# Optimization experiments

Measured on AMD Instinct MI355X. Metric: run time of the kernel, lower is better.

The kernel has to match this reference:

```python
import jax, jax.numpy as jnp
import numpy as np


def setup_inputs() -> dict:
    key = jax.random.key(0)
    ks = jax.random.split(key, 9)
    B, T, S, E, H = 4, 4096, 4096, 512, 64
    return {
        "x": jax.random.normal(ks[0], (B, T, 1), dtype=jnp.float32),
        "tok_emb": jax.random.normal(ks[1], (B, S, E), dtype=jnp.float32),
        "key_w": jax.random.normal(ks[2], (H, E), dtype=jnp.float32) * 0.05,
        "key_b": jax.random.normal(ks[3], (H,), dtype=jnp.float32) * 0.05,
        "query_w": jax.random.normal(ks[4], (H, 1), dtype=jnp.float32) * 0.05,
        "query_b": jax.random.normal(ks[5], (H,), dtype=jnp.float32) * 0.05,
        "value_w": jax.random.normal(ks[6], (H, E), dtype=jnp.float32) * 0.05,
        "proj_w": jax.random.normal(ks[7], (1, H), dtype=jnp.float32) * 0.05,
        "proj_b": jax.random.normal(ks[8], (1,), dtype=jnp.float32) * 0.05,
    }


def reference(x, tok_emb, key_w, key_b, query_w, query_b, value_w, proj_w, proj_b):
    # k = tanh(Linear(tok_emb))            [B,S,H]
    k = jnp.tanh(jnp.einsum("bse,he->bsh", tok_emb, key_w) + key_b)
    # q = tanh(Linear(x)); x last dim is 1 [B,T,H]
    q = jnp.tanh(jnp.einsum("btu,hu->bth", x, query_w) + query_b)
    scale = k.shape[-1] ** (-0.5)
    wei = jnp.einsum("bth,bsh->bts", q, k) * scale  # [B,T,S]
    # NOTE: softmax over dim=-2 (the query/T axis), faithful to the original
    wei = jax.nn.softmax(wei, axis=-2)
    v = jnp.tanh(jnp.einsum("bse,he->bsh", tok_emb, value_w))  # [B,S,H]
    out = jnp.tanh(jnp.einsum("bts,bsh->bth", wei, v))         # [B,T,H]
    out = jnp.einsum("bth,oh->bto", out, proj_w) + proj_b      # [B,T,1]
    return jnp.squeeze(out, axis=-1)                            # [B,T]
```

## Files before the change

### kernel.cpp

```cpp
#include <hip/hip_runtime.h>
#include <math.h>

#define BB 4
#define TT 4096
#define SS 4096
#define EE 512
#define HH 64
#define NN 128
#define XR 6.0f


typedef __attribute__((ext_vector_type(8))) __bf16 bf16x8;
typedef __attribute__((ext_vector_type(16))) float f32x16;

__device__ __forceinline__ unsigned short f2b(float f) {
  unsigned int u = __float_as_uint(f);
  return (unsigned short)((u + 0x7FFFu + ((u >> 16) & 1u)) >> 16);
}

__device__ __forceinline__ float fast_tanh(float v) {
  float e = __expf(fminf(60.0f, 2.0f * v));
  return (e - 1.0f) * __builtin_amdgcn_rcpf(e + 1.0f);
}

__global__ __launch_bounds__(256) void prep_sm_kernel(
    const float* __restrict__ kw, const float* __restrict__ vw,
    const float* __restrict__ qw, const float* __restrict__ qb,
    const float* __restrict__ x, unsigned int* __restrict__ Wfrag,
    float* __restrict__ Cmat, unsigned short* __restrict__ qnA,
    float* __restrict__ Sm_part, float* __restrict__ Oz) {
  const int blk = blockIdx.x;
  if (blk < 64) {
    int idx = blk * 256 + threadIdx.x;
    int jq = idx & 1;
    int l = (idx >> 1) & 63;
    int ks = (idx >> 7) & 31;
    int nb = idx >> 12;
    int n = nb * 32 + (l & 31);
    int k = ks * 16 + (l >> 5) * 8 + jq * 4;
    const float* row = (n < HH) ? (kw + n * EE + k) : (vw + (n - HH) * EE + k);
    float4 wv = *(const float4*)row;
    Wfrag[idx * 2] = (unsigned int)f2b(wv.x) | ((unsigned int)f2b(wv.y) << 16);
    Wfrag[idx * 2 + 1] =
        (unsigned int)f2b(wv.z) | ((unsigned int)f2b(wv.w) << 16);
  } else if (blk < 128) {
    int idx = (blk - 64) * 256 + threadIdx.x;
    int m = idx >> 7;
    int j = idx & (NN - 1);
    int k = (m * (2 * j + 1)) & 511;
    if (k >= 256) k -= 512;
    Cmat[idx] = cosf((float)k * (float)(M_PI / 256.0));
    if (idx < 8192) ((float4*)Oz)[idx] = make_float4(0.f, 0.f, 0.f, 0.f);
    if (idx < 8192) {
      int h = idx & 63;
      int j2 = idx >> 6;
      float th = (float)M_PI * ((float)j2 + 0.5f) * (1.0f / NN);
      float xj = XR * cosf(th);
      float val = tanhf(fmaf(xj, qw[h], qb[h]));
      int pos =
          (((j2 >> 5) * 4 + (h >> 4)) * 64 + (j2 & 31) + 32 * ((h >> 3) & 1)) *
              8 +
          (h & 7);
      qnA[pos] = f2b(val);
    }
  } else {
    __shared__ float Tm[128][NN + 1];
    int blk2 = blk - 128;
    int b = blk2 >> 5;
    int chunk = blk2 & 31;
    int tid = threadIdx.x;
    if (tid < 128) {
      float xh = x[b * TT + chunk * 128 + tid] * (1.0f / XR);
      xh = fminf(1.0f, fmaxf(-1.0f, xh));
      Tm[tid][0] = 1.0f;
      Tm[tid][1] = xh;
      float x2 = 2.0f * xh;
      float tm2 = 1.0f, tm1 = xh;
#pragma unroll 6
      for (int m = 2; m < NN; ++m) {
        float t = fmaf(x2, tm1, -tm2);
        Tm[tid][m] = t;
        tm2 = tm1;
        tm1 = t;
      }
    }
    __syncthreads();
    if (tid < 128) {
      float s = 0.f;
#pragma unroll 8
      for (int i = 0; i < 128; ++i) s += Tm[i][tid];
      Sm_part[(b * 32 + chunk) * NN + tid] = s;
    }
  }
}

__global__ __launch_bounds__(512) void kvattn_kernel(
    const float* __restrict__ emb, const float* __restrict__ kb,
    const unsigned int* __restrict__ Wfrag, const unsigned short* __restrict__ qnA,
    const float* __restrict__ Cmat, const float* __restrict__ Sm_part,
    float* __restrict__ O) {
  __shared__ __align__(16) char smem[69120];
  unsigned short* A_lds = (unsigned short*)smem;
  unsigned short* ktB = (unsigned short*)smem;
  unsigned short* vB = (unsigned short*)(smem + 8192);
  unsigned short* eA = (unsigned short*)(smem + 16384);
  float* zred = (float*)(smem + 65536);
  float* wql = (float*)(smem + 67840);
  float* izl = (float*)(smem + 68352);
  float* sml = (float*)(smem + 68608);

  const int tid = threadIdx.x;
  const int row0 = blockIdx.x * 64;
  const int bb = row0 >> 12;

  {
    int m = tid >> 3;
    int c8 = tid & 7;
    const float* src = emb + (size_t)(row0 + m) * EE;
    unsigned short* dst = A_lds + (m >> 5) * 16384;
    int ml = m & 31;
    float4 buf[16];
#pragma unroll
    for (int it = 0; it < 16; ++it)
      buf[it] = *(const float4*)(src + (c8 + it * 8) * 4);
#pragma unroll
    for (int it = 0; it < 16; ++it) {
      int k = (c8 + it * 8) * 4;
      float4 v = buf[it];
      int kstep = k >> 4;
      int lane_f = ml + 32 * ((k >> 3) & 1);
      int j = k & 7;
      unsigned int lo = (unsigned int)f2b(v.x) | ((unsigned int)f2b(v.y) << 16);
      unsigned int hi = (unsigned int)f2b(v.z) | ((unsigned int)f2b(v.w) << 16);
      *(uint2*)&dst[(kstep * 64 + lane_f) * 8 + j] = make_uint2(lo, hi);
    }
  }
  if (tid < 128) {
    float s = 0.f;
#pragma unroll 8
    for (int c = 0; c < 32; ++c) s += Sm_part[(bb * 32 + c) * NN + tid];
    sml[tid] = s * ((tid == 0) ? (1.0f / NN) : (2.0f / NN));
  }
  __syncthreads();
  if (tid < 128) {
    float a0 = 0.f, a1 = 0.f, a2 = 0.f, a3 = 0.f;
#pragma unroll
    for (int m = 0; m < NN; m += 4) {
      a0 = fmaf(sml[m], Cmat[m * NN + tid], a0);
      a1 = fmaf(sml[m + 1], Cmat[(m + 1) * NN + tid], a1);
      a2 = fmaf(sml[m + 2], Cmat[(m + 2) * NN + tid], a2);
      a3 = fmaf(sml[m + 3], Cmat[(m + 3) * NN + tid], a3);
    }
    wql[tid] = (a0 + a1) + (a2 + a3);
  }

  const int w8 = tid >> 6;
  const int lane = tid & 63;
  const int w = w8 & 3;
  const int mh = w8 >> 2;
  f32x16 acc = {};
  const bf16x8* Bf = (const bf16x8*)Wfrag;
  const unsigned short* Ah = A_lds + mh * 16384;
#pragma unroll 4
  for (int kstep = 0; kstep < 32; ++kstep) {
    bf16x8 bfr = Bf[(w * 32 + kstep) * 64 + lane];
    bf16x8 a = *(const bf16x8*)&Ah[(kstep * 64 + lane) * 8];
    acc = __builtin_amdgcn_mfma_f32_32x32x16_bf16(a, bfr, acc, 0, 0, 0);
  }
  __syncthreads();

  {
    const int n = w * 32 + (lane & 31);
    if (w < 2) {
      float kbv = kb[n];
      const int ks_h = n >> 4;
      const int off_h = 32 * ((n >> 3) & 1);
      const int jj_h = n & 7;
#pragma unroll
      for (int reg = 0; reg < 16; ++reg) {
        int sl = (reg & 3) + 8 * (reg >> 2) + 4 * (lane >> 5);
        ktB[((mh * 4 + ks_h) * 64 + sl + off_h) * 8 + jj_h] =
            f2b(fast_tanh(acc[reg] + kbv));
      }
    } else {
      int h = n - 64;
      const int nb_h = h >> 5;
      const int lm = h & 31;
#pragma unroll
      for (int reg = 0; reg < 16; ++reg) {
        int sl = (reg & 3) + 8 * (reg >> 2) + 4 * (lane >> 5);
        int s = mh * 32 + sl;
        vB[((nb_h * 4 + (s >> 4)) * 64 + lm + 32 * ((s >> 3) & 1)) * 8 +
           (s & 7)] = f2b(fast_tanh(acc[reg]));
      }
    }
  }
  __syncthreads();

  f32x16 l0 = {};
#pragma unroll
  for (int ks = 0; ks < 4; ++ks) {
    bf16x8 a = *(const bf16x8*)(qnA + ((w * 4 + ks) * 64 + lane) * 8);
    bf16x8 b0 = *(const bf16x8*)&ktB[((mh * 4 + ks) * 64 + lane) * 8];
    l0 = __builtin_amdgcn_mfma_f32_32x32x16_bf16(a, b0, l0, 0, 0, 0);
  }
  float e0[16];
  float zp = 0.f;
#pragma unroll
  for (int r = 0; r < 4; ++r) {
    float4 wq4 = *(const float4*)&wql[w * 32 + 8 * r + 4 * (lane >> 5)];
    float wa[4] = {wq4.x, wq4.y, wq4.z, wq4.w};
#pragma unroll
    for (int c = 0; c < 4; ++c) {
      int reg = 4 * r + c;
      e0[reg] = __expf(l0[reg] * 0.125f);
      zp = fmaf(wa[c], e0[reg], zp);
    }
  }
  zred[(mh * 32 + (lane & 31)) * 9 + w * 2 + (lane >> 5)] = zp;
  __syncthreads();
  if (tid < 64) {
    float sum = 0.f;
#pragma unroll
    for (int k = 0; k < 8; ++k) sum += zred[tid * 9 + k];
    izl[tid] = 1.0f / sum;
  }
  __syncthreads();

  {
    const int s = mh * 32 + (lane & 31);
    const float iz = izl[s];
    const int q0 = w * 4 + (s >> 4);
    const int lof = 32 * ((s >> 3) & 1);
    const int idx = s & 7;
#pragma unroll
    for (int reg = 0; reg < 16; ++reg) {
      int jl = (reg & 3) + 8 * (reg >> 2) + 4 * (lane >> 5);
      eA[(q0 * 64 + jl + lof) * 8 + idx] = f2b(e0[reg] * iz);
    }
  }
  __syncthreads();
  f32x16 o0 = {};
#pragma unroll
  for (int ks = 0; ks < 4; ++ks) {
    bf16x8 a = *(const bf16x8*)&eA[((w * 4 + ks) * 64 + lane) * 8];
    bf16x8 b0 = *(const bf16x8*)&vB[((mh * 4 + ks) * 64 + lane) * 8];
    o0 = __builtin_amdgcn_mfma_f32_32x32x16_bf16(a, b0, o0, 0, 0, 0);
  }
  float* op = O + (size_t)bb * (NN * HH);
  const int h0 = mh * 32 + (lane & 31);
#pragma unroll
  for (int reg = 0; reg < 16; ++reg) {
    int j = w * 32 + (reg & 3) + 8 * (reg >> 2) + 4 * (lane >> 5);
    atomicAdd(&op[j * HH + h0], o0[reg]);
  }
}

__global__ __launch_bounds__(256) void final_kernel(
    const float* __restrict__ x, const float* __restrict__ O,
    const float* __restrict__ pw, const float* __restrict__ pb,
    const float* __restrict__ Cmat, float* __restrict__ y) {
  const int idx = blockIdx.x * 256 + threadIdx.x;
  const int b = idx >> 12;
  __shared__ float yl[NN];
  __shared__ float c[NN];
  {
    const int j = threadIdx.x >> 1;
    const int half = threadIdx.x & 1;
    const float4* Ov =
        (const float4*)(O + ((size_t)(b * NN + j) * HH + half * 32));
    const float4* pwv = (const float4*)(pw + half * 32);
    float s = 0.f;
#pragma unroll
    for (int q = 0; q < 8; ++q) {
      float4 ov = Ov[q];
      float4 pv = pwv[q];
      s += fast_tanh(ov.x) * pv.x + fast_tanh(ov.y) * pv.y +
           fast_tanh(ov.z) * pv.z + fast_tanh(ov.w) * pv.w;
    }
    s += __shfl_xor(s, 1, 64);
    if (half == 0) yl[j] = s + pb[0];
  }
  __syncthreads();
  if (threadIdx.x < NN) {
    int m = threadIdx.x;
    double acc = 0.0;
#pragma unroll 8
    for (int j = 0; j < NN; ++j)
      acc += (double)yl[j] * (double)Cmat[m * NN + j];
    c[m] = (float)(acc * ((m == 0 ? 1.0 : 2.0) / NN));
  }
  __syncthreads();
  float xf = x[idx] * (1.0f / XR);
  xf = fminf(1.0f, fmaxf(-1.0f, xf));
  double xh = (double)xf;
  double b1 = 0.0, b2 = 0.0;
  for (int m = NN - 1; m >= 1; --m) {
    double t = fma(2.0 * xh, b1, (double)c[m] - b2);
    b2 = b1;
    b1 = t;
  }
  y[idx] = (float)fma(xh, b1, (double)c[0] - b2);
}

extern "C" void kernel_launch(void* const* d_in, const int* in_sizes, int n_in,
                              void* d_out, int out_size, void* d_ws,
                              size_t ws_size, hipStream_t stream) {
  const float* x = (const float*)d_in[0];
  const float* emb = (const float*)d_in[1];
  const float* kw = (const float*)d_in[2];
  const float* kb = (const float*)d_in[3];
  const float* qw = (const float*)d_in[4];
  const float* qb = (const float*)d_in[5];
  const float* vw = (const float*)d_in[6];
  const float* pw = (const float*)d_in[7];
  const float* pb = (const float*)d_in[8];

  float* ws = (float*)d_ws;
  float* O = ws;
  float* Cmat = ws + 32768;
  unsigned short* qnA = (unsigned short*)(Cmat + 16384);
  unsigned int* Wfrag = (unsigned int*)(Cmat + 16384 + 4096);
  float* Sm_part = (float*)(Wfrag + 32768);
  float* y = (float*)d_out;

  prep_sm_kernel<<<256, 256, 0, stream>>>(kw, vw, qw, qb, x, Wfrag, Cmat, qnA,
                                          Sm_part, O);
  kvattn_kernel<<<BB * SS / 64, 512, 0, stream>>>(emb, kb, Wfrag, qnA, Cmat,
                                                  Sm_part, O);
  final_kernel<<<BB * TT / 256, 256, 0, stream>>>(x, O, pw, pb, Cmat, y);
}
```

Baseline: 116.1 us.

## Fuse final Chebyshev evaluation into attention kernel via last-block counter

Removes the separate final kernel launch. Each attention block increments a per-batch completion counter, and the last block for each batch computes the projected values, the Chebyshev coefficients, and evaluates the series for all 4096 query positions. The series evaluation switches from double to float and uses an even/odd split in 2x^2-1, which halves the recurrence length. The trade-off is a serial tail run by only 4 blocks with 512 threads each, plus reduced precision in the evaluation.

Result: slower. 147.7 us (+27.3%).

```diff
diff --git a/kernel.cpp b/kernel.cpp
--- a/kernel.cpp
+++ b/kernel.cpp
@@ -28,7 +28,8 @@
     const float* __restrict__ qw, const float* __restrict__ qb,
     const float* __restrict__ x, unsigned int* __restrict__ Wfrag,
     float* __restrict__ Cmat, unsigned short* __restrict__ qnA,
-    float* __restrict__ Sm_part, float* __restrict__ Oz) {
+    float* __restrict__ Sm_part, float* __restrict__ Oz,
+    unsigned int* __restrict__ doneb) {
   const int blk = blockIdx.x;
   if (blk < 64) {
     int idx = blk * 256 + threadIdx.x;
@@ -63,6 +64,7 @@
           (h & 7);
       qnA[pos] = f2b(val);
     }
+    if (idx < 4) doneb[idx] = 0u;
   } else {
     __shared__ float Tm[128][NN + 1];
     int blk2 = blk - 128;
@@ -98,7 +100,9 @@
     const float* __restrict__ emb, const float* __restrict__ kb,
     const unsigned int* __restrict__ Wfrag, const unsigned short* __restrict__ qnA,
     const float* __restrict__ Cmat, const float* __restrict__ Sm_part,
-    float* __restrict__ O) {
+    float* __restrict__ O, const float* __restrict__ x,
+    const float* __restrict__ pw, const float* __restrict__ pb,
+    float* __restrict__ y, unsigned int* __restrict__ done) {
   __shared__ __align__(16) char smem[69120];
   unsigned short* A_lds = (unsigned short*)smem;
   unsigned short* ktB = (unsigned short*)smem;
@@ -254,53 +258,67 @@
     int j = w * 32 + (reg & 3) + 8 * (reg >> 2) + 4 * (lane >> 5);
     atomicAdd(&op[j * HH + h0], o0[reg]);
   }
-}
-
-__global__ __launch_bounds__(256) void final_kernel(
-    const float* __restrict__ x, const float* __restrict__ O,
-    const float* __restrict__ pw, const float* __restrict__ pb,
-    const float* __restrict__ Cmat, float* __restrict__ y) {
-  const int idx = blockIdx.x * 256 + threadIdx.x;
-  const int b = idx >> 12;
-  __shared__ float yl[NN];
-  __shared__ float c[NN];
+
+  __threadfence();
+  __syncthreads();
+  volatile unsigned* oldv = (volatile unsigned*)(smem + 65536);
+  if (tid == 0) *oldv = atomicAdd(&done[bb], 1u);
+  __syncthreads();
+  if (*oldv != 63u) return;
+  __threadfence();
+
+  float* yl = (float*)smem;
+  float* cc = (float*)(smem + 512);
+  if (tid < 128) {
+    const float* op2 = O + (size_t)bb * (NN * HH) + tid * HH;
+    float s = 0.f;
+#pragma unroll 8
+    for (int h = 0; h < HH; ++h) {
+      float ov = __hip_atomic_load(&op2[h], __ATOMIC_RELAXED,
+                                   __HIP_MEMORY_SCOPE_AGENT);
+      s = fmaf(fast_tanh(ov), pw[h], s);
+    }
+    yl[tid] = s + pb[0];
+  }
+  __syncthreads();
+  if (tid < 128) {
+    double a0 = 0.0, a1 = 0.0;
+#pragma unroll 4
+    for (int j = 0; j < NN; j += 2) {
+      a0 += (double)yl[j] * (double)Cmat[tid * NN + j];
+      a1 += (double)yl[j + 1] * (double)Cmat[tid * NN + j + 1];
+    }
+    cc[tid] = (float)((a0 + a1) * ((tid == 0 ? 1.0 : 2.0) / NN));
+  }
+  __syncthreads();
   {
-    const int j = threadIdx.x >> 1;
-    const int half = threadIdx.x & 1;
-    const float4* Ov =
-        (const float4*)(O + ((size_t)(b * NN + j) * HH + half * 32));
-    const float4* pwv = (const float4*)(pw + half * 32);
-    float s = 0.f;
-#pragma unroll
-    for (int q = 0; q < 8; ++q) {
-      float4 ov = Ov[q];
-      float4 pv = pwv[q];
-      s += fast_tanh(ov.x) * pv.x + fast_tanh(ov.y) * pv.y +
-           fast_tanh(ov.z) * pv.z + fast_tanh(ov.w) * pv.w;
-    }
-    s += __shfl_xor(s, 1, 64);
-    if (half == 0) yl[j] = s + pb[0];
-  }
-  __syncthreads();
-  if (threadIdx.x < NN) {
-    int m = threadIdx.x;
-    double acc = 0.0;
-#pragma unroll 8
-    for (int j = 0; j < NN; ++j)
-      acc += (double)yl[j] * (double)Cmat[m * NN + j];
-    c[m] = (float)(acc * ((m == 0 ? 1.0 : 2.0) / NN));
-  }
-  __syncthreads();
-  float xf = x[idx] * (1.0f / XR);
-  xf = fminf(1.0f, fmaxf(-1.0f, xf));
-  double xh = (double)xf;
-  double b1 = 0.0, b2 = 0.0;
-  for (int m = NN - 1; m >= 1; --m) {
-    double t = fma(2.0 * xh, b1, (double)c[m] - b2);
-    b2 = b1;
-    b1 = t;
-  }
-  y[idx] = (float)fma(xh, b1, (double)c[0] - b2);
+    float xf[8], uu[8], tu[8], be1[8], be2[8], bo1[8], bo2[8];
+#pragma unroll
+    for (int k = 0; k < 8; ++k) {
+      float xv = x[bb * TT + k * 512 + tid] * (1.0f / XR);
+      xv = fminf(1.0f, fmaxf(-1.0f, xv));
+      xf[k] = xv;
+      uu[k] = fmaf(2.0f * xv, xv, -1.0f);
+      tu[k] = 2.0f * uu[k];
+      be1[k] = be2[k] = bo1[k] = bo2[k] = 0.f;
+    }
+    for (int m = 63; m >= 0; --m) {
+      float ce = cc[2 * m], co = cc[2 * m + 1];
+#pragma unroll
+      for (int k = 0; k < 8; ++k) {
+        float be = fmaf(tu[k], be1[k], ce - be2[k]);
+        float bo = fmaf(tu[k], bo1[k], co - bo2[k]);
+        be2[k] = be1[k]; be1[k] = be;
+        bo2[k] = bo1[k]; bo1[k] = bo;
+      }
+    }
+#pragma unroll
+    for (int k = 0; k < 8; ++k) {
+      float fe = be1[k] - uu[k] * be2[k];
+      float fo = bo1[k] - bo2[k];
+      y[bb * TT + k * 512 + tid] = fmaf(xf[k], fo, fe);
+    }
+  }
 }
 
 extern "C" void kernel_launch(void* const* d_in, const int* in_sizes, int n_in,
@@ -322,11 +340,12 @@
   unsigned short* qnA = (unsigned short*)(Cmat + 16384);
   unsigned int* Wfrag = (unsigned int*)(Cmat + 16384 + 4096);
   float* Sm_part = (float*)(Wfrag + 32768);
+  unsigned int* done = (unsigned int*)(Sm_part + 16384);
   float* y = (float*)d_out;
 
   prep_sm_kernel<<<256, 256, 0, stream>>>(kw, vw, qw, qb, x, Wfrag, Cmat, qnA,
-                                          Sm_part, O);
+                                          Sm_part, O, done);
   kvattn_kernel<<<BB * SS / 64, 512, 0, stream>>>(emb, kb, Wfrag, qnA, Cmat,
-                                                  Sm_part, O);
-  final_kernel<<<BB * TT / 256, 256, 0, stream>>>(x, O, pw, pb, Cmat, y);
-}
+                                                  Sm_part, O, x, pw, pb, y,
+                                                  done);
+}
```
